# Optimization experiments

Hardware: AMD Instinct MI355X
Metric: run time of the kernel (lower is better)

The kernel has to match this reference:

```python
import jax, jax.numpy as jnp
import numpy as np
from jax import lax

T, B, D, H, C = 2048, 64, 128, 256, 5

def setup_inputs() -> dict:
    key = jax.random.key(0)
    k = jax.random.split(key, 7)
    s = 1.0 / np.sqrt(H)  # pytorch nn.RNN init scale
    return {
        "inputs": jax.random.normal(k[0], (T, B, D), dtype=jnp.float32),
        "W_ih": jax.random.uniform(k[1], (H, D), jnp.float32, -s, s),
        "W_hh": jax.random.uniform(k[2], (H, H), jnp.float32, -s, s),
        "b_ih": jax.random.uniform(k[3], (H,), jnp.float32, -s, s),
        "b_hh": jax.random.uniform(k[4], (H,), jnp.float32, -s, s),
        "W_fc": jax.random.uniform(k[5], (C, H), jnp.float32, -s, s),
        "b_fc": jax.random.uniform(k[6], (C,), jnp.float32, -s, s),
    }

def reference(inputs, W_ih, W_hh, b_ih, b_hh, W_fc, b_fc):
    # Precompute input projections for all timesteps: (T, B, H)
    x_proj = jnp.einsum('tbd,hd->tbh', inputs, W_ih) + b_ih + b_hh

    def step(h, xp):
        # h_t = tanh(W_ih x_t + b_ih + W_hh h_{t-1} + b_hh)
        h_new = jnp.tanh(xp + h @ W_hh.T)
        return h_new, None  # per-step outputs unused by the module head

    h0 = jnp.zeros((inputs.shape[1], W_hh.shape[0]), dtype=inputs.dtype)
    h_last, _ = lax.scan(step, h0, x_proj)

    logits = h_last @ W_fc.T + b_fc  # (B, 5)
    return jax.nn.log_softmax(logits, axis=1)
```

## Files before the change

### kernel.cpp

```cpp
#include <hip/hip_runtime.h>


#define T_DIM 2048
#define B_DIM 64
#define D_DIM 128
#define H_DIM 256
#define C_DIM 5

using floatx4 = __attribute__((ext_vector_type(4))) float;
using shortx8 = __attribute__((ext_vector_type(8))) short;

#define W_SCALE 2032.0f
#define H_SCALE 127.0f
#define INV_SCALE (1.0f / (2032.0f * 127.0f))
#define TWO_LOG2E 2.8853900817779268f
#define K_EXP (TWO_LOG2E * INV_SCALE)
#define MAGIC 12582912.0f

__device__ __forceinline__ short f2bf(float f) {
  unsigned int u = __float_as_uint(f);
  unsigned int r = (u + 0x7FFFu + ((u >> 16) & 1u)) >> 16;
  return (short)r;
}

__device__ __forceinline__ int sdot4(unsigned int a, unsigned int b, int c) {
#if __has_builtin(__builtin_amdgcn_sdot4)
  return __builtin_amdgcn_sdot4((int)a, (int)b, c, false);
#else
  int r = c;
  #pragma unroll
  for (int k = 0; k < 4; ++k)
    r += (int)(signed char)(a >> (8 * k)) * (int)(signed char)(b >> (8 * k));
  return r;
#endif
}

template<int CTRL>
__device__ __forceinline__ int dpp_movi(int x) {
  return __builtin_amdgcn_update_dpp(0, x, CTRL, 0xF, 0xF, true);
}

__device__ __forceinline__ float fast_exp2(float x) {
#if __has_builtin(__builtin_amdgcn_exp2f)
  return __builtin_amdgcn_exp2f(x);
#else
  return __exp2f(x);
#endif
}

__device__ __forceinline__ float fast_rcp(float x) {
#if __has_builtin(__builtin_amdgcn_rcpf)
  return __builtin_amdgcn_rcpf(x);
#else
  return __fdividef(1.0f, x);
#endif
}

__device__ __forceinline__ void barrier_lds_only() {
  asm volatile("s_waitcnt lgkmcnt(0)\n\ts_barrier" ::: "memory");
}

__device__ __forceinline__ void xp_body(
    const float* __restrict__ x,
    const float* __restrict__ W_ih,
    const float* __restrict__ b_ih,
    const float* __restrict__ b_hh,
    _Float16* __restrict__ xp,
    int cnt, int t0, int tstride, short* wlds)
{
  if (cnt <= 0) return;
  const int tid = threadIdx.x;
  {
    const int group = tid >> 2;
    const int sub = tid & 3;
    const int kf = group & 3;
    const int k0 = kf * 32 + sub * 8;
    #pragma unroll
    for (int i = 0; i < 16; ++i) {
      const int n = (group >> 2) * 16 + i;
      const float* src = W_ih + n * D_DIM + k0;
      float4 p0 = *(const float4*)(src);
      float4 p1 = *(const float4*)(src + 4);
      shortx8 v;
      v[0]=f2bf(p0.x); v[1]=f2bf(p0.y); v[2]=f2bf(p0.z); v[3]=f2bf(p0.w);
      v[4]=f2bf(p1.x); v[5]=f2bf(p1.y); v[6]=f2bf(p1.z); v[7]=f2bf(p1.w);
      *(shortx8*)&wlds[(group * 64 + sub * 16 + i) * 8] = v;
    }
  }
  __syncthreads();

  const int wv   = tid >> 6;
  const int lane = tid & 63;
  const int col  = lane & 15;
  const int quad = lane >> 4;

  float bias[16];
  #pragma unroll
  for (int nt = 0; nt < 16; ++nt)
    bias[nt] = b_ih[nt * 16 + col] + b_hh[nt * 16 + col];

  for (int t = t0; t < cnt; t += tstride) {
    const long m0 = (long)t * 64 + wv * 16;

    shortx8 af[4];
    const float* arow = x + (m0 + col) * D_DIM + quad * 8;
    #pragma unroll
    for (int kf = 0; kf < 4; ++kf) {
      float4 p0 = *(const float4*)(arow + kf * 32);
      float4 p1 = *(const float4*)(arow + kf * 32 + 4);
      shortx8 v;
      v[0]=f2bf(p0.x); v[1]=f2bf(p0.y); v[2]=f2bf(p0.z); v[3]=f2bf(p0.w);
      v[4]=f2bf(p1.x); v[5]=f2bf(p1.y); v[6]=f2bf(p1.z); v[7]=f2bf(p1.w);
      af[kf] = v;
    }

    #pragma unroll
    for (int nt = 0; nt < 16; ++nt) {
      floatx4 acc = {0.f, 0.f, 0.f, 0.f};
      #pragma unroll
      for (int kf = 0; kf < 4; ++kf) {
        shortx8 bfrag = *(const shortx8*)&wlds[((nt * 4 + kf) * 64 + lane) * 8];
        acc = __builtin_amdgcn_mfma_f32_16x16x32_bf16(af[kf], bfrag, acc, 0, 0, 0);
      }
      const int n = nt * 16 + col;
      #pragma unroll
      for (int r = 0; r < 4; ++r) {
        const long m = m0 + quad * 4 + r;
        xp[m * H_DIM + n] = (_Float16)(acc[r] + bias[nt]);
      }
    }
  }
}

__global__ __launch_bounds__(256) void xp_kernel(
    const float* __restrict__ x, const float* __restrict__ W_ih,
    const float* __restrict__ b_ih, const float* __restrict__ b_hh,
    _Float16* __restrict__ xp, int cnt)
{
  __shared__ __align__(16) short wlds[32768];
  xp_body(x, W_ih, b_ih, b_hh, xp, cnt, blockIdx.x, gridDim.x, wlds);
}

__global__ __launch_bounds__(256)
__attribute__((amdgpu_waves_per_eu(1, 1)))
void fused_kernel(
    const _Float16* __restrict__ xp,
    const float* __restrict__ W_hh,
    const float* __restrict__ W_fc,
    const float* __restrict__ b_fc,
    signed char* __restrict__ h8,
    float* __restrict__ out,
    int cnt, int first, int last,
    const float* __restrict__ x_next,
    const float* __restrict__ W_ih,
    const float* __restrict__ b_ih,
    const float* __restrict__ b_hh,
    _Float16* __restrict__ xp_next,
    int next_cnt)
{
  __shared__ __align__(16) short wlds[32768];
  __shared__ __align__(16) signed char hbuf[2][256];
  __shared__ float hfin[H_DIM];
  __shared__ float scratch[192];

  if (blockIdx.x >= 64) {
    xp_body(x_next, W_ih, b_ih, b_hh, xp_next, next_cnt,
            (int)blockIdx.x - 64, (int)gridDim.x - 64, wlds);
    return;
  }

  const int b   = blockIdx.x;
  const int tid = threadIdx.x;
  const int g   = tid >> 2;
  const int c   = tid & 3;

  unsigned int wq[4][16];
  const float* wbase = W_hh + (g * 4) * H_DIM + c * 64;
  #pragma unroll
  for (int r = 0; r < 4; ++r)
    #pragma unroll
    for (int i = 0; i < 16; ++i) {
      float4 f = *(const float4*)(wbase + r * H_DIM + i * 4);
      unsigned int q0 = (unsigned int)(int)rintf(f.x * W_SCALE) & 0xFFu;
      unsigned int q1 = (unsigned int)(int)rintf(f.y * W_SCALE) & 0xFFu;
      unsigned int q2 = (unsigned int)(int)rintf(f.z * W_SCALE) & 0xFFu;
      unsigned int q3 = (unsigned int)(int)rintf(f.w * W_SCALE) & 0xFFu;
      wq[r][i] = q0 | (q1 << 8) | (q2 << 16) | (q3 << 24);
    }
  #pragma unroll
  for (int r = 0; r < 4; ++r)
    #pragma unroll
    for (int i = 0; i < 16; ++i)
      asm volatile("" : "+v"(wq[r][i]));

  const int row_w = tid;
  hbuf[0][row_w] = first ? (signed char)0 : h8[b * H_DIM + row_w];
  __syncthreads();

  const size_t BH = (size_t)B_DIM * H_DIM;
  const _Float16* xpp = xp + (size_t)b * H_DIM + row_w;
  float hnlast = 0.f;

  auto step_body = [&](int bufsel, _Float16 xin) -> void {
    float xin2 = (float)xin * TWO_LOG2E;
    const signed char* hb = hbuf[bufsel] + c * 64;
    uint4 u0 = *(const uint4*)(hb);
    uint4 u1 = *(const uint4*)(hb + 16);
    uint4 u2 = *(const uint4*)(hb + 32);
    uint4 u3 = *(const uint4*)(hb + 48);
    const unsigned int hv[16] = {u0.x, u0.y, u0.z, u0.w, u1.x, u1.y, u1.z, u1.w,
                                 u2.x, u2.y, u2.z, u2.w, u3.x, u3.y, u3.z, u3.w};
    int a0l = 0, a1l = 0, a2l = 0, a3l = 0;
    int a0h = 0, a1h = 0, a2h = 0, a3h = 0;
    #pragma unroll
    for (int i = 0; i < 8; ++i) {
      a0l = sdot4(wq[0][i], hv[i], a0l);
      a1l = sdot4(wq[1][i], hv[i], a1l);
      a2l = sdot4(wq[2][i], hv[i], a2l);
      a3l = sdot4(wq[3][i], hv[i], a3l);
    }
    #pragma unroll
    for (int i = 8; i < 16; ++i) {
      a0h = sdot4(wq[0][i], hv[i], a0h);
      a1h = sdot4(wq[1][i], hv[i], a1h);
      a2h = sdot4(wq[2][i], hv[i], a2h);
      a3h = sdot4(wq[3][i], hv[i], a3h);
    }
    int a0 = a0l + a0h, a1 = a1l + a1h, a2 = a2l + a2h, a3 = a3l + a3h;
    int k01 = (c & 1) ? a1 : a0;
    int s01 = (c & 1) ? a0 : a1;
    int m0  = k01 + dpp_movi<0xB1>(s01);
    int k23 = (c & 1) ? a3 : a2;
    int s23 = (c & 1) ? a2 : a3;
    int m1  = k23 + dpp_movi<0xB1>(s23);
    int kk = (c & 2) ? m1 : m0;
    int sn = (c & 2) ? m0 : m1;
    int vi = kk + dpp_movi<0x4E>(sn);

    float arg = __builtin_fmaf((float)vi, K_EXP, xin2);
    float e   = fast_exp2(arg);
    float r   = fast_rcp(e + 1.0f);
    hnlast    = __builtin_fmaf(-254.0f, r, 127.0f);
    float qb  = __builtin_fmaf(-254.0f, r, MAGIC + 127.0f);
    hbuf[bufsel ^ 1][row_w] = (signed char)__float_as_int(qb);
    barrier_lds_only();
  };

  if ((cnt & 1) == 0 && cnt >= 2) {
    const _Float16* p = xpp;
    _Float16 x0 = p[0];
    _Float16 x1 = p[BH];
    for (int s = 0; s + 2 < cnt; s += 2) {
      step_body(0, x0); x0 = p[2 * BH];
      step_body(1, x1); x1 = p[3 * BH];
      p += 2 * BH;
    }
    step_body(0, x0);
    step_body(1, x1);
  } else {
    for (int s = 0; s < cnt; ++s)
      step_body(s & 1, xpp[(size_t)s * BH]);
  }

  h8[b * H_DIM + row_w] = hbuf[cnt & 1][row_w];

  if (last) {
    hfin[row_w] = hnlast * (1.0f / 127.0f);
    __syncthreads();
    if (tid < 160) {
      const int c5 = tid >> 5, i = tid & 31;
      float pp = 0.f;
      #pragma unroll
      for (int jj = 0; jj < 8; ++jj) {
        const int j = i * 8 + jj;
        pp += W_fc[c5 * H_DIM + j] * hfin[j];
      }
      scratch[tid] = pp;
    }
    __syncthreads();
    if (tid < C_DIM) {
      float l = b_fc[tid];
      for (int i = 0; i < 32; ++i) l += scratch[tid * 32 + i];
      scratch[160 + tid] = l;
    }
    __syncthreads();
    if (tid == 0) {
      float mx = scratch[160];
      for (int i = 1; i < C_DIM; ++i) mx = fmaxf(mx, scratch[160 + i]);
      float se = 0.f;
      for (int i = 0; i < C_DIM; ++i) se += __expf(scratch[160 + i] - mx);
      const float lse = mx + __logf(se);
      for (int i = 0; i < C_DIM; ++i) out[b * C_DIM + i] = scratch[160 + i] - lse;
    }
  }
}

extern "C" void kernel_launch(void* const* d_in, const int* in_sizes, int n_in,
                              void* d_out, int out_size, void* d_ws, size_t ws_size,
                              hipStream_t stream) {
  (void)in_sizes; (void)n_in; (void)out_size;
  const float* x    = (const float*)d_in[0];
  const float* W_ih = (const float*)d_in[1];
  const float* W_hh = (const float*)d_in[2];
  const float* b_ih = (const float*)d_in[3];
  const float* b_hh = (const float*)d_in[4];
  const float* W_fc = (const float*)d_in[5];
  const float* b_fc = (const float*)d_in[6];
  float* out = (float*)d_out;

  char* ws = (char*)d_ws;
  signed char* h8 = (signed char*)ws;
  _Float16* bufA = (_Float16*)(ws + 65536);
  const size_t step_bytes = (size_t)B_DIM * H_DIM * sizeof(_Float16);
  const size_t avail = ws_size > 65536 ? ws_size - 65536 : 0;
  const long cap2 = (long)(avail / (2 * step_bytes));

  if (cap2 >= 64) {
    long CAP = cap2 < 512 ? cap2 : 512;
    _Float16* bufB = bufA + (size_t)CAP * B_DIM * H_DIM;
    long bnd[64];
    bnd[0] = 0;
    long c0 = 256; if (c0 > CAP) c0 = CAP; if (c0 > T_DIM) c0 = T_DIM;
    bnd[1] = c0;
    int nc = 1;
    while (bnd[nc] < T_DIM && nc < 62) {
      long nx = bnd[nc] + CAP; if (nx > T_DIM) nx = T_DIM;
      bnd[nc + 1] = nx; ++nc;
    }
    {
      const unsigned gb = (unsigned)(c0 < 512 ? c0 : 512);
      xp_kernel<<<dim3(gb), dim3(256), 0, stream>>>(x, W_ih, b_ih, b_hh, bufA, (int)c0);
    }
    for (int k = 0; k < nc; ++k) {
      _Float16* src = (k & 1) ? bufB : bufA;
      _Float16* dst = (k & 1) ? bufA : bufB;
      const long s0 = bnd[k], s1 = bnd[k + 1];
      const int has_next = (k + 1 < nc) ? 1 : 0;
      const long n0 = has_next ? bnd[k + 1] : 0;
      const long n1 = has_next ? bnd[k + 2] : 0;
      fused_kernel<<<dim3(256), dim3(256), 0, stream>>>(
          src, W_hh, W_fc, b_fc, h8, out,
          (int)(s1 - s0), k == 0 ? 1 : 0, (k == nc - 1) ? 1 : 0,
          x + n0 * B_DIM * D_DIM, W_ih, b_ih, b_hh, dst, (int)(n1 - n0));
    }
  } else {
    long Tc = (long)(avail / step_bytes);
    if (Tc > T_DIM) Tc = T_DIM;
    if (Tc < 1) Tc = 1;
    for (long t0 = 0; t0 < T_DIM; t0 += Tc) {
      const long cnt = (T_DIM - t0 < Tc) ? (T_DIM - t0) : Tc;
      const unsigned gb = (unsigned)(cnt < 512 ? cnt : 512);
      xp_kernel<<<dim3(gb), dim3(256), 0, stream>>>(
          x + t0 * B_DIM * D_DIM, W_ih, b_ih, b_hh, bufA, (int)cnt);
      fused_kernel<<<dim3(64), dim3(256), 0, stream>>>(
          bufA, W_hh, W_fc, b_fc, h8, out,
          (int)cnt, t0 == 0 ? 1 : 0, (t0 + cnt == T_DIM) ? 1 : 0,
          x, W_ih, b_ih, b_hh, bufA, 0);
    }
  }
}
```

Baseline: 731.2 us.

## Assign one hidden row per thread in recurrence and vectorize xp conversion/stores

The recurrence kernel now has each thread hold a full 256-wide int8 row of W_hh and compute its dot product alone. This removes the DPP cross-lane reduction and per-lane selects, but each thread must read the whole h vector from LDS every step and keep 64 weight registers. The xp projection now uses the packed v_cvt_pk_bf16_f32 instruction and swaps the MFMA operands so each lane can write 4 contiguous fp16 outputs with vectorized bias. The chunk capacity also drops from 512 to 448 steps.

```diff
diff --git a/kernel.cpp b/kernel.cpp
--- a/kernel.cpp
+++ b/kernel.cpp
@@ -9,6 +9,7 @@
 
 using floatx4 = __attribute__((ext_vector_type(4))) float;
 using shortx8 = __attribute__((ext_vector_type(8))) short;
+using halfx4  = __attribute__((ext_vector_type(4))) _Float16;
 
 #define W_SCALE 2032.0f
 #define H_SCALE 127.0f
@@ -17,10 +18,19 @@
 #define K_EXP (TWO_LOG2E * INV_SCALE)
 #define MAGIC 12582912.0f
 
-__device__ __forceinline__ short f2bf(float f) {
-  unsigned int u = __float_as_uint(f);
-  unsigned int r = (u + 0x7FFFu + ((u >> 16) & 1u)) >> 16;
-  return (short)r;
+__device__ __forceinline__ unsigned int cvt_pk_bf16(float lo, float hi) {
+  unsigned int d;
+  asm("v_cvt_pk_bf16_f32 %0, %1, %2" : "=v"(d) : "v"(lo), "v"(hi));
+  return d;
+}
+
+__device__ __forceinline__ shortx8 pack_bf16x8(float4 p0, float4 p1) {
+  union { unsigned int u[4]; shortx8 v; } r;
+  r.u[0] = cvt_pk_bf16(p0.x, p0.y);
+  r.u[1] = cvt_pk_bf16(p0.z, p0.w);
+  r.u[2] = cvt_pk_bf16(p1.x, p1.y);
+  r.u[3] = cvt_pk_bf16(p1.z, p1.w);
+  return r.v;
 }
 
 __device__ __forceinline__ int sdot4(unsigned int a, unsigned int b, int c) {
@@ -33,11 +43,6 @@
     r += (int)(signed char)(a >> (8 * k)) * (int)(signed char)(b >> (8 * k));
   return r;
 #endif
-}
-
-template<int CTRL>
-__device__ __forceinline__ int dpp_movi(int x) {
-  return __builtin_amdgcn_update_dpp(0, x, CTRL, 0xF, 0xF, true);
 }
 
 __device__ __forceinline__ float fast_exp2(float x) {
@@ -79,12 +84,8 @@
     for (int i = 0; i < 16; ++i) {
       const int n = (group >> 2) * 16 + i;
       const float* src = W_ih + n * D_DIM + k0;
-      float4 p0 = *(const float4*)(src);
-      float4 p1 = *(const float4*)(src + 4);
-      shortx8 v;
-      v[0]=f2bf(p0.x); v[1]=f2bf(p0.y); v[2]=f2bf(p0.z); v[3]=f2bf(p0.w);
-      v[4]=f2bf(p1.x); v[5]=f2bf(p1.y); v[6]=f2bf(p1.z); v[7]=f2bf(p1.w);
-      *(shortx8*)&wlds[(group * 64 + sub * 16 + i) * 8] = v;
+      *(shortx8*)&wlds[(group * 64 + sub * 16 + i) * 8] =
+          pack_bf16x8(*(const float4*)(src), *(const float4*)(src + 4));
     }
   }
   __syncthreads();
@@ -94,10 +95,14 @@
   const int col  = lane & 15;
   const int quad = lane >> 4;
 
-  float bias[16];
+  float4 bias4[16];
   #pragma unroll
-  for (int nt = 0; nt < 16; ++nt)
-    bias[nt] = b_ih[nt * 16 + col] + b_hh[nt * 16 + col];
+  for (int nt = 0; nt < 16; ++nt) {
+    const int nb = nt * 16 + quad * 4;
+    float4 bi = *(const float4*)(b_ih + nb);
+    float4 bh = *(const float4*)(b_hh + nb);
+    bias4[nt] = make_float4(bi.x + bh.x, bi.y + bh.y, bi.z + bh.z, bi.w + bh.w);
+  }
 
   for (int t = t0; t < cnt; t += tstride) {
     const long m0 = (long)t * 64 + wv * 16;
@@ -105,29 +110,25 @@
     shortx8 af[4];
     const float* arow = x + (m0 + col) * D_DIM + quad * 8;
     #pragma unroll
-    for (int kf = 0; kf < 4; ++kf) {
-      float4 p0 = *(const float4*)(arow + kf * 32);
-      float4 p1 = *(const float4*)(arow + kf * 32 + 4);
-      shortx8 v;
-      v[0]=f2bf(p0.x); v[1]=f2bf(p0.y); v[2]=f2bf(p0.z); v[3]=f2bf(p0.w);
-      v[4]=f2bf(p1.x); v[5]=f2bf(p1.y); v[6]=f2bf(p1.z); v[7]=f2bf(p1.w);
-      af[kf] = v;
-    }
-
+    for (int kf = 0; kf < 4; ++kf)
+      af[kf] = pack_bf16x8(*(const float4*)(arow + kf * 32),
+                           *(const float4*)(arow + kf * 32 + 4));
+
+    _Float16* orow = xp + (m0 + col) * H_DIM + quad * 4;
     #pragma unroll
     for (int nt = 0; nt < 16; ++nt) {
       floatx4 acc = {0.f, 0.f, 0.f, 0.f};
       #pragma unroll
       for (int kf = 0; kf < 4; ++kf) {
-        shortx8 bfrag = *(const shortx8*)&wlds[((nt * 4 + kf) * 64 + lane) * 8];
-        acc = __builtin_amdgcn_mfma_f32_16x16x32_bf16(af[kf], bfrag, acc, 0, 0, 0);
+        shortx8 wfrag = *(const shortx8*)&wlds[((nt * 4 + kf) * 64 + lane) * 8];
+        acc = __builtin_amdgcn_mfma_f32_16x16x32_bf16(wfrag, af[kf], acc, 0, 0, 0);
       }
-      const int n = nt * 16 + col;
-      #pragma unroll
-      for (int r = 0; r < 4; ++r) {
-        const long m = m0 + quad * 4 + r;
-        xp[m * H_DIM + n] = (_Float16)(acc[r] + bias[nt]);
-      }
+      halfx4 v;
+      v[0] = (_Float16)(acc[0] + bias4[nt].x);
+      v[1] = (_Float16)(acc[1] + bias4[nt].y);
+      v[2] = (_Float16)(acc[2] + bias4[nt].z);
+      v[3] = (_Float16)(acc[3] + bias4[nt].w);
+      *(halfx4*)(orow + nt * 16) = v;
     }
   }
 }
@@ -171,78 +172,59 @@
 
   const int b   = blockIdx.x;
   const int tid = threadIdx.x;
-  const int g   = tid >> 2;
-  const int c   = tid & 3;
-
-  unsigned int wq[4][16];
-  const float* wbase = W_hh + (g * 4) * H_DIM + c * 64;
+
+  unsigned int wq[64];
+  const float* wrow = W_hh + tid * H_DIM;
   #pragma unroll
-  for (int r = 0; r < 4; ++r)
+  for (int i = 0; i < 64; ++i) {
+    float4 f = *(const float4*)(wrow + i * 4);
+    unsigned int q0 = (unsigned int)(int)rintf(f.x * W_SCALE) & 0xFFu;
+    unsigned int q1 = (unsigned int)(int)rintf(f.y * W_SCALE) & 0xFFu;
+    unsigned int q2 = (unsigned int)(int)rintf(f.z * W_SCALE) & 0xFFu;
+    unsigned int q3 = (unsigned int)(int)rintf(f.w * W_SCALE) & 0xFFu;
+    wq[i] = q0 | (q1 << 8) | (q2 << 16) | (q3 << 24);
+  }
+  #pragma unroll
+  for (int i = 0; i < 64; ++i)
+    asm volatile("" : "+v"(wq[i]));
+
+  hbuf[0][tid] = first ? (signed char)0 : h8[b * H_DIM + tid];
+  __syncthreads();
+
+  const size_t BH = (size_t)B_DIM * H_DIM;
+  const _Float16* xpp = xp + (size_t)b * H_DIM + tid;
+  float hnlast = 0.f;
+
+  auto step_body = [&](int bufsel, _Float16 xin) -> void {
+    float x2 = (float)xin * TWO_LOG2E;
+    const uint4* hb4 = (const uint4*)hbuf[bufsel];
+    unsigned int hv[64];
     #pragma unroll
     for (int i = 0; i < 16; ++i) {
-      float4 f = *(const float4*)(wbase + r * H_DIM + i * 4);
-      unsigned int q0 = (unsigned int)(int)rintf(f.x * W_SCALE) & 0xFFu;
-      unsigned int q1 = (unsigned int)(int)rintf(f.y * W_SCALE) & 0xFFu;
-      unsigned int q2 = (unsigned int)(int)rintf(f.z * W_SCALE) & 0xFFu;
-      unsigned int q3 = (unsigned int)(int)rintf(f.w * W_SCALE) & 0xFFu;
-      wq[r][i] = q0 | (q1 << 8) | (q2 << 16) | (q3 << 24);
-    }
-  #pragma unroll
-  for (int r = 0; r < 4; ++r)
-    #pragma unroll
-    for (int i = 0; i < 16; ++i)
-      asm volatile("" : "+v"(wq[r][i]));
-
-  const int row_w = tid;
-  hbuf[0][row_w] = first ? (signed char)0 : h8[b * H_DIM + row_w];
-  __syncthreads();
-
-  const size_t BH = (size_t)B_DIM * H_DIM;
-  const _Float16* xpp = xp + (size_t)b * H_DIM + row_w;
-  float hnlast = 0.f;
-
-  auto step_body = [&](int bufsel, _Float16 xin) -> void {
-    float xin2 = (float)xin * TWO_LOG2E;
-    const signed char* hb = hbuf[bufsel] + c * 64;
-    uint4 u0 = *(const uint4*)(hb);
-    uint4 u1 = *(const uint4*)(hb + 16);
-    uint4 u2 = *(const uint4*)(hb + 32);
-    uint4 u3 = *(const uint4*)(hb + 48);
-    const unsigned int hv[16] = {u0.x, u0.y, u0.z, u0.w, u1.x, u1.y, u1.z, u1.w,
-                                 u2.x, u2.y, u2.z, u2.w, u3.x, u3.y, u3.z, u3.w};
-    int a0l = 0, a1l = 0, a2l = 0, a3l = 0;
-    int a0h = 0, a1h = 0, a2h = 0, a3h = 0;
-    #pragma unroll
-    for (int i = 0; i < 8; ++i) {
-      a0l = sdot4(wq[0][i], hv[i], a0l);
-      a1l = sdot4(wq[1][i], hv[i], a1l);
-      a2l = sdot4(wq[2][i], hv[i], a2l);
-      a3l = sdot4(wq[3][i], hv[i], a3l);
-    }
-    #pragma unroll
-    for (int i = 8; i < 16; ++i) {
-      a0h = sdot4(wq[0][i], hv[i], a0h);
-      a1h = sdot4(wq[1][i], hv[i], a1h);
-      a2h = sdot4(wq[2][i], hv[i], a2h);
-      a3h = sdot4(wq[3][i], hv[i], a3h);
-    }
-    int a0 = a0l + a0h, a1 = a1l + a1h, a2 = a2l + a2h, a3 = a3l + a3h;
-    int k01 = (c & 1) ? a1 : a0;
-    int s01 = (c & 1) ? a0 : a1;
-    int m0  = k01 + dpp_movi<0xB1>(s01);
-    int k23 = (c & 1) ? a3 : a2;
-    int s23 = (c & 1) ? a2 : a3;
-    int m1  = k23 + dpp_movi<0xB1>(s23);
-    int kk = (c & 2) ? m1 : m0;
-    int sn = (c & 2) ? m0 : m1;
-    int vi = kk + dpp_movi<0x4E>(sn);
-
-    float arg = __builtin_fmaf((float)vi, K_EXP, xin2);
+      uint4 q = hb4[i];
+      hv[4 * i + 0] = q.x; hv[4 * i + 1] = q.y;
+      hv[4 * i + 2] = q.z; hv[4 * i + 3] = q.w;
+    }
+    int a0 = 0, a1 = 0, a2 = 0, a3 = 0, a4 = 0, a5 = 0, a6 = 0, a7 = 0;
+    #pragma unroll
+    for (int j = 0; j < 8; ++j) {
+      a0 = sdot4(wq[j * 8 + 0], hv[j * 8 + 0], a0);
+      a1 = sdot4(wq[j * 8 + 1], hv[j * 8 + 1], a1);
+      a2 = sdot4(wq[j * 8 + 2], hv[j * 8 + 2], a2);
+      a3 = sdot4(wq[j * 8 + 3], hv[j * 8 + 3], a3);
+      a4 = sdot4(wq[j * 8 + 4], hv[j * 8 + 4], a4);
+      a5 = sdot4(wq[j * 8 + 5], hv[j * 8 + 5], a5);
+      a6 = sdot4(wq[j * 8 + 6], hv[j * 8 + 6], a6);
+      a7 = sdot4(wq[j * 8 + 7], hv[j * 8 + 7], a7);
+    }
+    int vi = ((a0 + a1) + (a2 + a3)) + ((a4 + a5) + (a6 + a7));
+
+    float arg = __builtin_fmaf((float)vi, K_EXP, x2);
     float e   = fast_exp2(arg);
     float r   = fast_rcp(e + 1.0f);
     hnlast    = __builtin_fmaf(-254.0f, r, 127.0f);
     float qb  = __builtin_fmaf(-254.0f, r, MAGIC + 127.0f);
-    hbuf[bufsel ^ 1][row_w] = (signed char)__float_as_int(qb);
+    hbuf[bufsel ^ 1][tid] = (signed char)__float_as_int(qb);
     barrier_lds_only();
   };
 
@@ -262,10 +244,10 @@
       step_body(s & 1, xpp[(size_t)s * BH]);
   }
 
-  h8[b * H_DIM + row_w] = hbuf[cnt & 1][row_w];
+  h8[b * H_DIM + tid] = hbuf[cnt & 1][tid];
 
   if (last) {
-    hfin[row_w] = hnlast * (1.0f / 127.0f);
+    hfin[tid] = hnlast * (1.0f / 127.0f);
     __syncthreads();
     if (tid < 160) {
       const int c5 = tid >> 5, i = tid & 31;
@@ -316,7 +298,7 @@
   const long cap2 = (long)(avail / (2 * step_bytes));
 
   if (cap2 >= 64) {
-    long CAP = cap2 < 512 ? cap2 : 512;
+    long CAP = cap2 < 448 ? cap2 : 448;
     _Float16* bufB = bufA + (size_t)CAP * B_DIM * H_DIM;
     long bnd[64];
     bnd[0] = 0;
```

Result: slower. 857.5 us (+17.3%).
